# Kernel optimization log

Measured on AMD Instinct MI355X. Metric: run time of the kernel, lower is better.

The kernel has to match this reference:

```python
import jax, jax.numpy as jnp
import numpy as np

# SLAYER neuron / simulation hyperparameters (from network.yaml)
THETA = 10.0      # spike threshold
TAU_SR = 10.0     # SRM (PSP) kernel time constant [ms]
TAU_REF = 1.0     # refractory kernel time constant [ms]
SCALE_REF = 2.0   # refractory kernel scale
TS = 1.0          # simulation step [ms]
K_SRM = 100       # truncation length of SRM kernel (eps decays ~0 by 10*tau)
K_REF = 32        # truncation length of refractory kernel (tauRef=1 -> decays fast)


def _eps_kernel(tau, k):
    # eps(t) = (t/tau) * exp(1 - t/tau), eps(0) = 0  (SLAYER SRM alpha kernel)
    t = jnp.arange(k, dtype=jnp.float32) * TS
    return (t / tau) * jnp.exp(1.0 - t / tau)


def psp(x, kern):
    # Causal temporal filter: y[..., t] = sum_j kern[j] * x[..., t - j]
    B, N, T = x.shape
    lhs = x.reshape(B * N, 1, T)
    rhs = kern[::-1].reshape(1, 1, -1)  # lax.conv is cross-correlation -> flip
    y = jax.lax.conv_general_dilated(
        lhs, rhs, window_strides=(1,), padding=[(kern.shape[0] - 1, 0)],
        dimension_numbers=('NCH', 'OIH', 'NCH'))
    return y.reshape(B, N, T)


def spike(u, refk):
    # Sequential thresholding with refractory feedback (SLAYER spikeFunction fwd).
    # u: [B, N, T] membrane drive. State r: future refractory contributions.
    kr = refk.shape[0]
    refk_shift = jnp.concatenate([refk[1:], jnp.zeros((1,), refk.dtype)])

    def step(r, u_t):
        m = u_t + r[..., 0]                      # membrane potential at t
        s = (m >= THETA).astype(u_t.dtype)       # hard spike
        r_next = jnp.concatenate([r[..., 1:], jnp.zeros_like(r[..., :1])], -1) \
                 + s[..., None] * refk_shift     # add refractory response
        return r_next, s

    uT = jnp.moveaxis(u, -1, 0)                  # [T, B, N]
    r0 = jnp.zeros(uT.shape[1:] + (kr,), u.dtype)
    _, sT = jax.lax.scan(step, r0, uT)
    return jnp.moveaxis(sT, 0, -1) / TS          # [B, N, T]


def setup_inputs() -> dict:
    key = jax.random.key(0)
    k1, k2, k3 = jax.random.split(key, 3)
    B, NIN, NHID, NOUT, T = 32, 2048, 512, 10, 350
    spike_input = (jax.random.uniform(k1, (B, NIN, T)) < 0.05).astype(jnp.float32)
    W1 = jax.random.normal(k2, (NHID, NIN), dtype=jnp.float32) * 0.05
    W2 = jax.random.normal(k3, (NOUT, NHID), dtype=jnp.float32) * 0.05
    return {"spike_input": spike_input, "W1": W1, "W2": W2}


def reference(spike_input, W1, W2):
    srm = _eps_kernel(TAU_SR, K_SRM)
    refk = -SCALE_REF * THETA * _eps_kernel(TAU_REF, K_REF)
    # layer 1: psp -> dense -> spike
    a1 = jnp.einsum('bnt,mn->bmt', psp(spike_input, srm), W1)
    s1 = spike(a1, refk)
    # layer 2: psp -> dense -> spike
    a2 = jnp.einsum('bnt,mn->bmt', psp(s1, srm), W2)
    s2 = spike(a2, refk)
    return s2
```

## Files before the change

### kernel.cpp

```cpp
#include <hip/hip_runtime.h>
#include <stdint.h>

static constexpr int B  = 32;
static constexpr int T  = 350;
static constexpr int NIN = 2048;
static constexpr int NH  = 512;
static constexpr int NO  = 10;
static constexpr int BT  = B * T;

static constexpr float THETA = 10.0f;
static constexpr float BETA  = 0.36787944117144233f;
static constexpr float CREF  = 54.365636569180904707f;

static constexpr size_t OFF_W1TS = 0;
static constexpr size_t OFF_MASK = 4196352;
static constexpr size_t OFF_SRM  = 7080960;
static constexpr size_t OFF_Z1   = 7081984;
static constexpr size_t OFF_A1   = 30019584;
static constexpr size_t OFF_LST  = OFF_A1;
static constexpr size_t OFF_CNT  = OFF_A1 + 4300800;
static constexpr size_t OFF_Z2   = OFF_Z1;

static constexpr int SLICE_F = 8;
static constexpr int NSLICE  = NH / SLICE_F;
static constexpr int SLICE_STRIDE = 2049 * SLICE_F;

__global__ void __launch_bounds__(256) k_prep(const float* __restrict__ x,
                                              const float* __restrict__ W1,
                                              float* __restrict__ W1Ts,
                                              uint64_t* __restrict__ mask,
                                              float* __restrict__ srm28) {
    int bid = blockIdx.x;
    if (bid < 1024) {
        __shared__ uint64_t tb[6][64];
        int b = bid >> 5, nblk = bid & 31;
        int wv = threadIdx.x >> 6, lane = threadIdx.x & 63;
        for (int g = 0; g < 4; ++g) {
            float v[4][6];
            #pragma unroll
            for (int i = 0; i < 4; ++i) {
                int nr = wv + 4 * (4 * g + i);
                const float* xp = x + ((size_t)b * NIN + nblk * 64 + nr) * T;
                #pragma unroll
                for (int c = 0; c < 6; ++c) {
                    int t = c * 64 + lane;
                    v[i][c] = (t < T) ? xp[t] : 0.f;
                }
            }
            #pragma unroll
            for (int i = 0; i < 4; ++i) {
                int nr = wv + 4 * (4 * g + i);
                #pragma unroll
                for (int c = 0; c < 6; ++c) {
                    uint64_t mk = __ballot(v[i][c] != 0.0f);
                    if (lane == 0) tb[c][nr] = mk;
                }
            }
        }
        __syncthreads();
        static const uint64_t AM[6] = {
            0x00000000FFFFFFFFull, 0x0000FFFF0000FFFFull, 0x00FF00FF00FF00FFull,
            0x0F0F0F0F0F0F0F0Full, 0x3333333333333333ull, 0x5555555555555555ull };
        for (int c = wv; c < 6; c += 4) {
            uint64_t w = tb[c][lane];
            #pragma unroll
            for (int i = 0; i < 6; ++i) {
                int s = 32 >> i;
                uint64_t A = AM[i];
                uint64_t y = __shfl_xor((unsigned long long)w, s);
                if ((lane & s) == 0) w = (w & A)  | ((y & A) << s);
                else                 w = (w & ~A) | ((y & ~A) >> s);
            }
            int t = c * 64 + lane;
            if (t < T) mask[((size_t)b * 32 + nblk) * 352 + t] = w;
        }
    } else if (bid < 2048) {
        __shared__ float tile[32][33];
        int idx = bid - 1024;
        int n0 = (idx & 63) * 32, m0 = (idx >> 6) * 32;
        int tx = threadIdx.x & 31, ty0 = threadIdx.x >> 5;
        #pragma unroll
        for (int i = 0; i < 4; ++i) {
            int ty = ty0 + 8 * i;
            tile[ty][tx] = W1[(size_t)(m0 + ty) * NIN + n0 + tx];
        }
        __syncthreads();
        #pragma unroll
        for (int i = 0; i < 4; ++i) {
            int ty = ty0 + 8 * i;
            int n = n0 + ty, m = m0 + tx;
            W1Ts[(size_t)(m >> 3) * SLICE_STRIDE + n * SLICE_F + (m & 7)] = tile[tx][ty];
        }
    } else {
        int j = threadIdx.x;
        if (j < 192) {
            float v = 0.f;
            int i = j - 28;
            if (i >= 0 && i < 100) { float t = (float)i; v = (t * 0.1f) * expf(1.f - t * 0.1f); }
            srm28[j] = v;
        }
        for (int i = j; i < NSLICE * SLICE_F; i += 256)
            W1Ts[(size_t)(i >> 3) * SLICE_STRIDE + 2048 * SLICE_F + (i & 7)] = 0.f;
    }
}

__global__ void __launch_bounds__(64) k_decode(const uint64_t* __restrict__ mask,
                                               uint16_t* __restrict__ glst,
                                               int* __restrict__ gcnt) {
    __shared__ uint16_t lst[192];
    int t = blockIdx.x, b = blockIdx.y;
    int row = b * T + t;
    int lane = threadIdx.x;
    uint64_t w = (lane < 32) ? mask[((size_t)b * 32 + lane) * 352 + t] : 0ull;
    int cnt = __popcll(w);
    int pre = cnt;
    #pragma unroll
    for (int off = 1; off < 64; off <<= 1) {
        int v = __shfl_up(pre, off);
        if (lane >= off) pre += v;
    }
    int total = __shfl(pre, 63);
    int excl = pre - cnt;
    while (w) {
        int bit = __builtin_ctzll(w);
        w &= w - 1;
        lst[excl++] = (uint16_t)((lane << 6) + bit);
    }
    int padded = (total + 7) & ~7;
    if (lane < padded - total) lst[total + lane] = 2048;
    __syncthreads();
    uint16_t* op = glst + (size_t)row * 192;
    for (int i = lane; i < padded; i += 64) op[i] = lst[i];
    if (lane == 0) gcnt[row] = padded;
}

__global__ void __launch_bounds__(256) k_z1s(const uint16_t* __restrict__ glst,
                                             const int* __restrict__ gcnt,
                                             const float* __restrict__ W1Ts,
                                             float* __restrict__ z1) {
    __shared__ float w1s[SLICE_STRIDE];
    int s = blockIdx.x;
    int bt0 = blockIdx.y * (BT / 8);
    const float4* src = (const float4*)(W1Ts + (size_t)s * SLICE_STRIDE);
    for (int i = threadIdx.x; i < SLICE_STRIDE / 4; i += 256)
        ((float4*)w1s)[i] = src[i];
    __syncthreads();

    int q  = threadIdx.x & 1;
    int rl = threadIdx.x >> 1;
    for (int rr = rl; rr < BT / 8; rr += 128) {
        int row = bt0 + rr;
        int padded = gcnt[row];
        const ushort4* lp = (const ushort4*)(glst + (size_t)row * 192);
        float4 acc = {0, 0, 0, 0};
        for (int k = 0; k < padded; k += 8) {
            ushort4 q0 = lp[k >> 2];
            ushort4 q1 = lp[(k >> 2) + 1];
            const float* base = w1s + q * 4;
            float4 x0 = *(const float4*)(base + q0.x * SLICE_F);
            float4 x1 = *(const float4*)(base + q0.y * SLICE_F);
            float4 x2 = *(const float4*)(base + q0.z * SLICE_F);
            float4 x3 = *(const float4*)(base + q0.w * SLICE_F);
            float4 x4 = *(const float4*)(base + q1.x * SLICE_F);
            float4 x5 = *(const float4*)(base + q1.y * SLICE_F);
            float4 x6 = *(const float4*)(base + q1.z * SLICE_F);
            float4 x7 = *(const float4*)(base + q1.w * SLICE_F);
            acc.x += x0.x; acc.y += x0.y; acc.z += x0.z; acc.w += x0.w;
            acc.x += x1.x; acc.y += x1.y; acc.z += x1.z; acc.w += x1.w;
            acc.x += x2.x; acc.y += x2.y; acc.z += x2.z; acc.w += x2.w;
            acc.x += x3.x; acc.y += x3.y; acc.z += x3.z; acc.w += x3.w;
            acc.x += x4.x; acc.y += x4.y; acc.z += x4.z; acc.w += x4.w;
            acc.x += x5.x; acc.y += x5.y; acc.z += x5.z; acc.w += x5.w;
            acc.x += x6.x; acc.y += x6.y; acc.z += x6.z; acc.w += x6.w;
            acc.x += x7.x; acc.y += x7.y; acc.z += x7.z; acc.w += x7.w;
        }
        *(float4*)(z1 + (size_t)row * NH + s * SLICE_F + q * 4) = acc;
    }
}

__global__ void __launch_bounds__(64) k_fir1(const float* __restrict__ src,
                                             float* __restrict__ dst,
                                             const float* __restrict__ srm28) {
    __shared__ float tb[192];
    int b = blockIdx.x, half = blockIdx.y, tg = blockIdx.z;
    int lane = threadIdx.x;
    for (int i = lane; i < 192; i += 64) tb[i] = srm28[i];
    __syncthreads();
    int t0 = tg * 16;
    int m = half * 256 + lane * 4;
    const float* sp = src + (size_t)b * T * NH + m;

    float4 acc[16];
    #pragma unroll
    for (int r = 0; r < 16; ++r) acc[r] = make_float4(0.f, 0.f, 0.f, 0.f);
    float c[16];
    #pragma unroll
    for (int r = 0; r < 16; ++r) c[r] = tb[r + 127];

    for (int o = 0; o < 8; ++o) {
        #pragma unroll
        for (int j = 0; j < 16; ++j) {
            int dd = o * 16 + j;
            int tau = t0 - 99 + dd;
            float4 v = make_float4(0.f, 0.f, 0.f, 0.f);
            if (tau >= 0 && tau < T) v = *(const float4*)(sp + (size_t)tau * NH);
            #pragma unroll
            for (int r = 0; r < 16; ++r) {
                acc[r].x += c[r] * v.x; acc[r].y += c[r] * v.y;
                acc[r].z += c[r] * v.z; acc[r].w += c[r] * v.w;
            }
            #pragma unroll
            for (int r = 15; r > 0; --r) c[r] = c[r - 1];
            int ci = 126 - dd;
            c[0] = tb[ci < 0 ? 0 : ci];
        }
    }
    #pragma unroll
    for (int r = 0; r < 16; ++r) {
        int t = t0 + r;
        if (t < T) *(float4*)(dst + ((size_t)b * T + t) * NH + m) = acc[r];
    }
}

__global__ void __launch_bounds__(512) k_scanz2(const float* __restrict__ a1,
                                                const float* __restrict__ W2,
                                                float* __restrict__ z2) {
    __shared__ float w2s[NO * NH];
    __shared__ uint64_t smask[16][8];
    constexpr int CT = 16;
    constexpr int NC = (T + CT - 1) / CT;
    int b = blockIdx.x, tid = threadIdx.x;
    int wv = tid >> 6;
    for (int i = tid; i < NO * NH; i += 512) w2s[i] = W2[i];
    const float* up = a1 + (size_t)b * T * NH + tid;
    float A = 0.f, Bs = 0.f;
    float cur[CT], nxt[CT];
    #pragma unroll
    for (int j = 0; j < CT; ++j) cur[j] = up[(size_t)j * NH];
    __syncthreads();
    for (int c = 0; c < NC; ++c) {
        int t0 = c * CT;
        int nsteps = (T - t0 < CT) ? (T - t0) : CT;
        if (c + 1 < NC) {
            #pragma unroll
            for (int j = 0; j < CT; ++j) {
                int t = t0 + CT + j;
                nxt[j] = (t < T) ? up[(size_t)t * NH] : 0.f;
            }
        }
        #pragma unroll
        for (int j = 0; j < CT; ++j) {
            if (j < nsteps) {
                float mem = cur[j] - CREF * Bs;
                float sp = (mem >= THETA) ? 1.0f : 0.0f;
                A = sp + BETA * A;
                Bs = BETA * (Bs + A);
                uint64_t mk = __ballot(sp != 0.0f);
                if ((tid & 63) == 0) smask[j][wv] = mk;
            }
        }
        __syncthreads();
        if (tid < nsteps * NO) {
            int j = tid / NO, o = tid - j * NO;
            const float* wrow = w2s + o * NH;
            float acc = 0.f;
            #pragma unroll
            for (int w8 = 0; w8 < 8; ++w8) {
                uint64_t mk = smask[j][w8];
                int base = w8 * 64;
                while (mk) {
                    int bit = __builtin_ctzll(mk);
                    mk &= mk - 1;
                    acc += wrow[base + bit];
                }
            }
            z2[((size_t)b * T + t0 + j) * NO + o] = acc;
        }
        __syncthreads();
        #pragma unroll
        for (int j = 0; j < CT; ++j) cur[j] = nxt[j];
    }
}

__global__ void __launch_bounds__(256) k_fir2scan(const float* __restrict__ z2,
                                                  const float* __restrict__ srm28,
                                                  float* __restrict__ out) {
    __shared__ float tb[192];
    __shared__ float zb[350 * 11 + 16];
    __shared__ float ab[352 * 10];
    int b = blockIdx.x, tid = threadIdx.x;
    if (tid < 192) tb[tid] = srm28[tid];
    const float* zp = z2 + (size_t)b * T * NO;
    for (int i = tid; i < T * NO; i += 256) {
        int t = i / NO, o = i - t * NO;
        zb[t * 11 + o] = zp[i];
    }
    __syncthreads();
    if (tid < 220) {
        int tt = tid / 10, o = tid - tt * 10;
        int t0 = tt * 16;
        float acc[16];
        #pragma unroll
        for (int r = 0; r < 16; ++r) acc[r] = 0.f;
        float c[16];
        #pragma unroll
        for (int r = 0; r < 16; ++r) c[r] = tb[r + 127];
        for (int oo = 0; oo < 8; ++oo) {
            #pragma unroll
            for (int j = 0; j < 16; ++j) {
                int dd = oo * 16 + j;
                int tau = t0 - 99 + dd;
                float v = (tau >= 0 && tau < T) ? zb[tau * 11 + o] : 0.f;
                #pragma unroll
                for (int r = 0; r < 16; ++r) acc[r] += c[r] * v;
                #pragma unroll
                for (int r = 15; r > 0; --r) c[r] = c[r - 1];
                int ci = 126 - dd;
                c[0] = tb[ci < 0 ? 0 : ci];
            }
        }
        #pragma unroll
        for (int r = 0; r < 16; ++r) {
            int t = t0 + r;
            if (t < T) ab[t * 10 + o] = acc[r];
        }
    }
    __syncthreads();
    if (tid < NO) {
        int o = tid;
        float A = 0.f, Bs = 0.f;
        float* op = out + ((size_t)b * NO + o) * T;
        for (int t = 0; t < T; ++t) {
            float mem = ab[t * 10 + o] - CREF * Bs;
            float sp = (mem >= THETA) ? 1.0f : 0.0f;
            A = sp + BETA * A;
            Bs = BETA * (Bs + A);
            op[t] = sp;
        }
    }
}

extern "C" void kernel_launch(void* const* d_in, const int* in_sizes, int n_in,
                              void* d_out, int out_size, void* d_ws, size_t ws_size,
                              hipStream_t stream) {
    const float* x  = (const float*)d_in[0];
    const float* W1 = (const float*)d_in[1];
    const float* W2 = (const float*)d_in[2];
    char* ws = (char*)d_ws;
    float*    W1Ts = (float*)(ws + OFF_W1TS);
    uint64_t* mask = (uint64_t*)(ws + OFF_MASK);
    float*    srm  = (float*)(ws + OFF_SRM);
    float*    z1   = (float*)(ws + OFF_Z1);
    float*    a1   = (float*)(ws + OFF_A1);
    uint16_t* glst = (uint16_t*)(ws + OFF_LST);
    int*      gcnt = (int*)(ws + OFF_CNT);
    float*    z2   = (float*)(ws + OFF_Z2);
    float*    out  = (float*)d_out;

    hipLaunchKernelGGL(k_prep,       dim3(2049),      dim3(256), 0, stream, x, W1, W1Ts, mask, srm);
    hipLaunchKernelGGL(k_decode,     dim3(T, B),      dim3(64),  0, stream, mask, glst, gcnt);
    hipLaunchKernelGGL(k_z1s,        dim3(NSLICE, 8), dim3(256), 0, stream, glst, gcnt, W1Ts, z1);
    hipLaunchKernelGGL(k_fir1,       dim3(B, 2, 22),  dim3(64),  0, stream, z1, a1, srm);
    hipLaunchKernelGGL(k_scanz2,     dim3(B),         dim3(512), 0, stream, a1, W2, z2);
    hipLaunchKernelGGL(k_fir2scan,   dim3(B),         dim3(256), 0, stream, z2, srm, out);
}
```

Baseline: 310.5 us.

## Fuse spike-mask decode into prep and merge layer-2 scan with FIR/scan

The input bitmask build and the sparse index-list decode are merged into one prep stage. Each block now handles a batch and a 64-step time chunk, transposes the ballot masks in shared memory and writes the index lists directly, so the separate decode launch and the global mask buffer go away. The layer-2 dense/scan kernel and the final FIR+spike kernel are also fused, with z2 kept in shared memory instead of round-tripping through global memory. This removes two launches and some traffic, but prep now runs only 192 mask blocks, each serially decoding 64 rows, and k_l2 uses more shared memory per block, which could lengthen the critical path.

```diff
diff --git a/kernel.cpp b/kernel.cpp
--- a/kernel.cpp
+++ b/kernel.cpp
@@ -13,13 +13,11 @@
 static constexpr float CREF  = 54.365636569180904707f;
 
 static constexpr size_t OFF_W1TS = 0;
-static constexpr size_t OFF_MASK = 4196352;
-static constexpr size_t OFF_SRM  = 7080960;
-static constexpr size_t OFF_Z1   = 7081984;
-static constexpr size_t OFF_A1   = 30019584;
+static constexpr size_t OFF_SRM  = 4196352;
+static constexpr size_t OFF_Z1   = 4197376;
+static constexpr size_t OFF_A1   = 27134976;
 static constexpr size_t OFF_LST  = OFF_A1;
 static constexpr size_t OFF_CNT  = OFF_A1 + 4300800;
-static constexpr size_t OFF_Z2   = OFF_Z1;
 
 static constexpr int SLICE_F = 8;
 static constexpr int NSLICE  = NH / SLICE_F;
@@ -28,41 +26,38 @@
 __global__ void __launch_bounds__(256) k_prep(const float* __restrict__ x,
                                               const float* __restrict__ W1,
                                               float* __restrict__ W1Ts,
-                                              uint64_t* __restrict__ mask,
+                                              uint16_t* __restrict__ glst,
+                                              int* __restrict__ gcnt,
                                               float* __restrict__ srm28) {
     int bid = blockIdx.x;
-    if (bid < 1024) {
-        __shared__ uint64_t tb[6][64];
-        int b = bid >> 5, nblk = bid & 31;
+    if (bid < 192) {
+        __shared__ uint64_t mw[2048];
+        __shared__ uint64_t arr[64][33];
+        __shared__ uint16_t lstb[4][200];
+        int b = bid / 6, tc = bid % 6;
         int wv = threadIdx.x >> 6, lane = threadIdx.x & 63;
-        for (int g = 0; g < 4; ++g) {
-            float v[4][6];
-            #pragma unroll
-            for (int i = 0; i < 4; ++i) {
-                int nr = wv + 4 * (4 * g + i);
-                const float* xp = x + ((size_t)b * NIN + nblk * 64 + nr) * T;
-                #pragma unroll
-                for (int c = 0; c < 6; ++c) {
-                    int t = c * 64 + lane;
-                    v[i][c] = (t < T) ? xp[t] : 0.f;
-                }
-            }
-            #pragma unroll
-            for (int i = 0; i < 4; ++i) {
-                int nr = wv + 4 * (4 * g + i);
-                #pragma unroll
-                for (int c = 0; c < 6; ++c) {
-                    uint64_t mk = __ballot(v[i][c] != 0.0f);
-                    if (lane == 0) tb[c][nr] = mk;
-                }
+        int tbase = tc * 64;
+        int t_l = tbase + lane;
+        for (int g = 0; g < 32; ++g) {
+            int n0 = wv * 512 + g * 16;
+            float v[16];
+            #pragma unroll
+            for (int i = 0; i < 16; ++i) {
+                const float* xp = x + ((size_t)b * NIN + n0 + i) * T;
+                v[i] = (t_l < T) ? xp[t_l] : 0.f;
+            }
+            #pragma unroll
+            for (int i = 0; i < 16; ++i) {
+                uint64_t mk = __ballot(v[i] != 0.0f);
+                if (lane == 0) mw[n0 + i] = mk;
             }
         }
         __syncthreads();
         static const uint64_t AM[6] = {
             0x00000000FFFFFFFFull, 0x0000FFFF0000FFFFull, 0x00FF00FF00FF00FFull,
             0x0F0F0F0F0F0F0F0Full, 0x3333333333333333ull, 0x5555555555555555ull };
-        for (int c = wv; c < 6; c += 4) {
-            uint64_t w = tb[c][lane];
+        for (int g = wv; g < 32; g += 4) {
+            uint64_t w = mw[g * 64 + lane];
             #pragma unroll
             for (int i = 0; i < 6; ++i) {
                 int s = 32 >> i;
@@ -71,12 +66,39 @@
                 if ((lane & s) == 0) w = (w & A)  | ((y & A) << s);
                 else                 w = (w & ~A) | ((y & ~A) >> s);
             }
-            int t = c * 64 + lane;
-            if (t < T) mask[((size_t)b * 32 + nblk) * 352 + t] = w;
-        }
-    } else if (bid < 2048) {
+            arr[lane][g] = w;
+        }
+        __syncthreads();
+        for (int r = 0; r < 16; ++r) {
+            int tl = wv * 16 + r;
+            int t = tbase + tl;
+            if (t >= T) continue;
+            int row = b * T + t;
+            uint64_t w = (lane < 32) ? arr[tl][lane] : 0ull;
+            int cnt = __popcll(w);
+            int pre = cnt;
+            #pragma unroll
+            for (int off = 1; off < 64; off <<= 1) {
+                int v = __shfl_up(pre, off);
+                if (lane >= off) pre += v;
+            }
+            int total = __shfl(pre, 63);
+            int excl = pre - cnt;
+            uint16_t* lst = lstb[wv];
+            while (w) {
+                int bit = __builtin_ctzll(w);
+                w &= w - 1;
+                lst[excl++] = (uint16_t)((lane << 6) + bit);
+            }
+            int padded = (total + 7) & ~7;
+            if (lane < padded - total) lst[total + lane] = 2048;
+            uint16_t* op = glst + (size_t)row * 192;
+            for (int i = lane; i < padded; i += 64) op[i] = lst[i];
+            if (lane == 0) gcnt[row] = padded;
+        }
+    } else if (bid < 1216) {
         __shared__ float tile[32][33];
-        int idx = bid - 1024;
+        int idx = bid - 192;
         int n0 = (idx & 63) * 32, m0 = (idx >> 6) * 32;
         int tx = threadIdx.x & 31, ty0 = threadIdx.x >> 5;
         #pragma unroll
@@ -102,36 +124,6 @@
         for (int i = j; i < NSLICE * SLICE_F; i += 256)
             W1Ts[(size_t)(i >> 3) * SLICE_STRIDE + 2048 * SLICE_F + (i & 7)] = 0.f;
     }
-}
-
-__global__ void __launch_bounds__(64) k_decode(const uint64_t* __restrict__ mask,
-                                               uint16_t* __restrict__ glst,
-                                               int* __restrict__ gcnt) {
-    __shared__ uint16_t lst[192];
-    int t = blockIdx.x, b = blockIdx.y;
-    int row = b * T + t;
-    int lane = threadIdx.x;
-    uint64_t w = (lane < 32) ? mask[((size_t)b * 32 + lane) * 352 + t] : 0ull;
-    int cnt = __popcll(w);
-    int pre = cnt;
-    #pragma unroll
-    for (int off = 1; off < 64; off <<= 1) {
-        int v = __shfl_up(pre, off);
-        if (lane >= off) pre += v;
-    }
-    int total = __shfl(pre, 63);
-    int excl = pre - cnt;
-    while (w) {
-        int bit = __builtin_ctzll(w);
-        w &= w - 1;
-        lst[excl++] = (uint16_t)((lane << 6) + bit);
-    }
-    int padded = (total + 7) & ~7;
-    if (lane < padded - total) lst[total + lane] = 2048;
-    __syncthreads();
-    uint16_t* op = glst + (size_t)row * 192;
-    for (int i = lane; i < padded; i += 64) op[i] = lst[i];
-    if (lane == 0) gcnt[row] = padded;
 }
 
 __global__ void __launch_bounds__(256) k_z1s(const uint16_t* __restrict__ glst,
@@ -222,16 +214,21 @@
     }
 }
 
-__global__ void __launch_bounds__(512) k_scanz2(const float* __restrict__ a1,
-                                                const float* __restrict__ W2,
-                                                float* __restrict__ z2) {
+__global__ void __launch_bounds__(512) k_l2(const float* __restrict__ a1,
+                                            const float* __restrict__ W2,
+                                            const float* __restrict__ srm28,
+                                            float* __restrict__ out) {
     __shared__ float w2s[NO * NH];
     __shared__ uint64_t smask[16][8];
+    __shared__ float tb[192];
+    __shared__ float zb[350 * 11 + 16];
+    __shared__ float ab[352 * 10];
     constexpr int CT = 16;
     constexpr int NC = (T + CT - 1) / CT;
     int b = blockIdx.x, tid = threadIdx.x;
     int wv = tid >> 6;
     for (int i = tid; i < NO * NH; i += 512) w2s[i] = W2[i];
+    if (tid < 192) tb[tid] = srm28[tid];
     const float* up = a1 + (size_t)b * T * NH + tid;
     float A = 0.f, Bs = 0.f;
     float cur[CT], nxt[CT];
@@ -274,26 +271,11 @@
                     acc += wrow[base + bit];
                 }
             }
-            z2[((size_t)b * T + t0 + j) * NO + o] = acc;
+            zb[(t0 + j) * 11 + o] = acc;
         }
         __syncthreads();
         #pragma unroll
         for (int j = 0; j < CT; ++j) cur[j] = nxt[j];
-    }
-}
-
-__global__ void __launch_bounds__(256) k_fir2scan(const float* __restrict__ z2,
-                                                  const float* __restrict__ srm28,
-                                                  float* __restrict__ out) {
-    __shared__ float tb[192];
-    __shared__ float zb[350 * 11 + 16];
-    __shared__ float ab[352 * 10];
-    int b = blockIdx.x, tid = threadIdx.x;
-    if (tid < 192) tb[tid] = srm28[tid];
-    const float* zp = z2 + (size_t)b * T * NO;
-    for (int i = tid; i < T * NO; i += 256) {
-        int t = i / NO, o = i - t * NO;
-        zb[t * 11 + o] = zp[i];
     }
     __syncthreads();
     if (tid < 220) {
@@ -328,13 +310,13 @@
     __syncthreads();
     if (tid < NO) {
         int o = tid;
-        float A = 0.f, Bs = 0.f;
+        float A2 = 0.f, B2 = 0.f;
         float* op = out + ((size_t)b * NO + o) * T;
         for (int t = 0; t < T; ++t) {
-            float mem = ab[t * 10 + o] - CREF * Bs;
+            float mem = ab[t * 10 + o] - CREF * B2;
             float sp = (mem >= THETA) ? 1.0f : 0.0f;
-            A = sp + BETA * A;
-            Bs = BETA * (Bs + A);
+            A2 = sp + BETA * A2;
+            B2 = BETA * (B2 + A2);
             op[t] = sp;
         }
     }
@@ -348,19 +330,15 @@
     const float* W2 = (const float*)d_in[2];
     char* ws = (char*)d_ws;
     float*    W1Ts = (float*)(ws + OFF_W1TS);
-    uint64_t* mask = (uint64_t*)(ws + OFF_MASK);
     float*    srm  = (float*)(ws + OFF_SRM);
     float*    z1   = (float*)(ws + OFF_Z1);
     float*    a1   = (float*)(ws + OFF_A1);
     uint16_t* glst = (uint16_t*)(ws + OFF_LST);
     int*      gcnt = (int*)(ws + OFF_CNT);
-    float*    z2   = (float*)(ws + OFF_Z2);
     float*    out  = (float*)d_out;
 
-    hipLaunchKernelGGL(k_prep,       dim3(2049),      dim3(256), 0, stream, x, W1, W1Ts, mask, srm);
-    hipLaunchKernelGGL(k_decode,     dim3(T, B),      dim3(64),  0, stream, mask, glst, gcnt);
-    hipLaunchKernelGGL(k_z1s,        dim3(NSLICE, 8), dim3(256), 0, stream, glst, gcnt, W1Ts, z1);
-    hipLaunchKernelGGL(k_fir1,       dim3(B, 2, 22),  dim3(64),  0, stream, z1, a1, srm);
-    hipLaunchKernelGGL(k_scanz2,     dim3(B),         dim3(512), 0, stream, a1, W2, z2);
-    hipLaunchKernelGGL(k_fir2scan,   dim3(B),         dim3(256), 0, stream, z2, srm, out);
-}
+    hipLaunchKernelGGL(k_prep, dim3(1217),      dim3(256), 0, stream, x, W1, W1Ts, glst, gcnt, srm);
+    hipLaunchKernelGGL(k_z1s,  dim3(NSLICE, 8), dim3(256), 0, stream, glst, gcnt, W1Ts, z1);
+    hipLaunchKernelGGL(k_fir1, dim3(B, 2, 22),  dim3(64),  0, stream, z1, a1, srm);
+    hipLaunchKernelGGL(k_l2,   dim3(B),         dim3(512), 0, stream, a1, W2, srm, out);
+}
```

Result: slower. 584.5 us (+88.3%).
